# Optimization experiments

Measured on AMD Instinct MI355X. Metric: run time of the kernel, lower is better.

The kernel has to match this reference:

```python
import jax, jax.numpy as jnp
import numpy as np

BUCKETS = 16


def conv2d(x, w, b):
    # x: [N, Cin, H, W], w: [Cout, Cin, kh, kw], stride 1, padding 1
    y = jax.lax.conv_general_dilated(
        x, w, window_strides=(1, 1), padding=((1, 1), (1, 1)),
        dimension_numbers=("NCHW", "OIHW", "NCHW"))
    return y + b[None, :, None, None]


def setup_inputs() -> dict:
    key = jax.random.key(0)
    k1, k2, k3, k4, k5 = jax.random.split(key, 5)
    x = jax.random.normal(k1, (32, 64, 112, 112), dtype=jnp.float32)
    W = jax.random.normal(k2, (128, 64, 3, 3), dtype=jnp.float32) * 0.05
    b = jax.random.normal(k3, (128,), dtype=jnp.float32) * 0.05
    b2 = jax.random.normal(k4, (128,), dtype=jnp.float32) * 0.05  # hashed_conv's own bias
    hashed_weights = jax.random.normal(k5, (BUCKETS,), dtype=jnp.float32)
    return {"x": x, "W": W, "b": b, "b2": b2, "hashed_weights": hashed_weights}


def reference(x, W, b, b2, hashed_weights):
    out = conv2d(x, W, b)
    # thresholds derived from min/max of the ORIGINAL weights
    wmax = jnp.max(W)
    wmin = jnp.min(W)
    step = (wmax - wmin) / BUCKETS
    # sequential per-bucket replacement (faithful to in-place loop semantics:
    # values replaced at bucket i are re-compared against later thresholds)
    hw = W
    for i in range(BUCKETS):
        thr = (i + 1) * step + wmin
        hw = jnp.where(hw > thr, hashed_weights[i], hw)
    hashed_out = conv2d(x, hw, b2)
    return (out, hashed_out)
```

## Files before the change

### kernel.cpp

```cpp
#include <hip/hip_runtime.h>
#include <stdint.h>

#define CIN 64
#define HHW 112
#define NPIX 12544
#define COUT 128
#define KTOT 576
#define NBUCKETS 16

typedef __attribute__((ext_vector_type(8))) short s8v;
typedef __attribute__((ext_vector_type(4))) float f4v;
typedef __attribute__((ext_vector_type(8))) unsigned short u8v;

__device__ __forceinline__ unsigned short f2bf(float f) {
  unsigned int u = __float_as_uint(f);
  unsigned int r = (u + 0x7fffu + ((u >> 16) & 1u)) >> 16;
  return (unsigned short)r;
}

__device__ __forceinline__ void gload_lds16(const void* g, void* l) {
  __builtin_amdgcn_global_load_lds(
      (const __attribute__((address_space(1))) unsigned int*)g,
      (__attribute__((address_space(3))) unsigned int*)l, 16, 0, 0);
}

__global__ __launch_bounds__(1024) void hashedconv_prep_kernel(
    const float* __restrict__ W, const float* __restrict__ hashed_w,
    unsigned short* __restrict__ W2) {
  const int NW = COUT * CIN * 9;
  int tid = threadIdx.x;
  float vmin = 1e30f, vmax = -1e30f;
  for (int i = tid; i < NW; i += 1024) {
    float v = W[i];
    vmin = fminf(vmin, v);
    vmax = fmaxf(vmax, v);
  }
  #pragma unroll
  for (int off = 32; off > 0; off >>= 1) {
    vmin = fminf(vmin, __shfl_down(vmin, off, 64));
    vmax = fmaxf(vmax, __shfl_down(vmax, off, 64));
  }
  __shared__ float smin[16], smax[16];
  __shared__ float s_wmin, s_step;
  __shared__ float hv[NBUCKETS];
  int wave = tid >> 6, lane = tid & 63;
  if (lane == 0) { smin[wave] = vmin; smax[wave] = vmax; }
  if (tid < NBUCKETS) hv[tid] = hashed_w[tid];
  __syncthreads();
  if (tid == 0) {
    float m = smin[0], M = smax[0];
    #pragma unroll
    for (int i = 1; i < 16; ++i) { m = fminf(m, smin[i]); M = fmaxf(M, smax[i]); }
    s_wmin = m;
    s_step = (M - m) / (float)NBUCKETS;
  }
  __syncthreads();
  float wmin = s_wmin, step = s_step;
  for (int i = tid; i < NW; i += 1024) {
    float v = W[i];
    int co  = i / 576;
    int rem = i - co * 576;
    int cin = rem / 9;
    int off = rem - cin * 9;
    float h = v;
    #pragma unroll
    for (int b = 0; b < NBUCKETS; ++b) {
      float thr = (float)(b + 1) * step + wmin;
      if (h > thr) h = hv[b];
    }
    int oidx = co * KTOT + off * 64 + cin;
    W2[oidx]               = f2bf(v);
    W2[COUT * KTOT + oidx] = f2bf(h);
  }
}

__global__ __launch_bounds__(256) void xpose_kernel(
    const float* __restrict__ x, unsigned short* __restrict__ xb) {
  __shared__ unsigned short t[64][264];
  const int n = blockIdx.y, p0 = blockIdx.x * 256, tid = threadIdx.x;
  const float* xp = x + (size_t)n * CIN * NPIX + p0;
  #pragma unroll
  for (int c = 0; c < 64; ++c)
    t[c][tid] = f2bf(xp[(size_t)c * NPIX + tid]);
  __syncthreads();
  unsigned short* ob = xb + ((size_t)n * NPIX + p0) * 64;
  #pragma unroll
  for (int it = 0; it < 8; ++it) {
    int u = it * 256 + tid;
    int px = u >> 3, slot = u & 7;
    u8v v;
    #pragma unroll
    for (int k = 0; k < 8; ++k) v[k] = t[slot * 8 + k][px];
    *(u8v*)(ob + (size_t)u * 8) = v;
  }
}

#define XS_PIXPAD 352
#define XS_SHORTS (XS_PIXPAD * 64)
#define WS_SHORTS (COUT * 64)

__global__ __launch_bounds__(256, 2) void hashedconv_mfma_kernel(
    const unsigned short* __restrict__ xb, const unsigned short* __restrict__ W2,
    const float* __restrict__ b, const float* __restrict__ b2,
    const unsigned short* __restrict__ zp, float* __restrict__ out,
    size_t out_half) {
  __shared__ __attribute__((aligned(16))) short lds[XS_SHORTS + 2 * WS_SHORTS];
  short* xs = lds;
  short* ws0 = lds + XS_SHORTS;

  const int tid = threadIdx.x;
  const int bx = blockIdx.x;
  const int n  = blockIdx.y;
  const int hf = blockIdx.z;
  const int ty = bx / 7, tx = bx - ty * 7;
  const int h0 = ty * 16, w0 = tx * 16;
  const int lane = tid & 63, wv = tid >> 6;
  const int wr = wv >> 1, wcn = wv & 1;
  const int lrow = lane & 15, g = lane >> 4;

  const unsigned short* Wh = W2 + (size_t)hf * COUT * KTOT;

  #pragma unroll
  for (int it = 0; it < 11; ++it) {
    int u = it * 256 + tid;
    int pix = u >> 3, slot = u & 7;
    int py = pix / 18, px = pix - py * 18;
    int gh = h0 - 1 + py, gw = w0 - 1 + px;
    bool inb = (pix < 324) & (gh >= 0) & (gh < HHW) & (gw >= 0) & (gw < HHW);
    int srcslot = slot ^ (pix & 7);
    const unsigned short* gsrc = inb
        ? xb + (((size_t)n * NPIX + gh * HHW + gw) * 64 + srcslot * 8)
        : zp + srcslot * 8;
    gload_lds16(gsrc, xs + (size_t)(it * 256 + wv * 64) * 8);
  }

  auto stage_w = [&](short* buf, int c) {
    #pragma unroll
    for (int j = 0; j < 4; ++j) {
      int u = j * 256 + tid;
      int row = u >> 3, slot = u & 7;
      int srcslot = slot ^ (row & 7);
      gload_lds16(Wh + (size_t)row * KTOT + c * 64 + srcslot * 8,
                  buf + (size_t)(j * 256 + wv * 64) * 8);
    }
  };

  f4v acc[4][8];
  #pragma unroll
  for (int i = 0; i < 4; ++i)
    #pragma unroll
    for (int j = 0; j < 8; ++j) acc[i][j] = (f4v)(0.f);

  int pyv[8], pxv[8];
  #pragma unroll
  for (int nt = 0; nt < 8; ++nt) {
    int p = wcn * 128 + nt * 16 + lrow;
    pyv[nt] = p >> 4; pxv[nt] = p & 15;
  }

  stage_w(ws0, 0);
  __syncthreads();

  int cur = 0;
  for (int c = 0; c < 9; ++c) {
    short* wbuf = ws0 + cur * WS_SHORTS;
    if (c < 8) stage_w(ws0 + (cur ^ 1) * WS_SHORTS, c + 1);
    int dh = c / 3, dw = c - dh * 3;
    #pragma unroll
    for (int kh2 = 0; kh2 < 2; ++kh2) {
      int kofs = kh2 * 32 + g * 8;
      s8v af[4], bfv[8];
      #pragma unroll
      for (int mt = 0; mt < 4; ++mt) {
        int row = wr * 64 + mt * 16 + lrow;
        af[mt] = *(const s8v*)(wbuf + row * 64 + (kofs ^ ((row & 7) << 3)));
      }
      #pragma unroll
      for (int nt = 0; nt < 8; ++nt) {
        int s = (pyv[nt] + dh) * 18 + pxv[nt] + dw;
        bfv[nt] = *(const s8v*)(xs + s * 64 + (kofs ^ ((s & 7) << 3)));
      }
      #pragma unroll
      for (int mt = 0; mt < 4; ++mt)
        #pragma unroll
        for (int nt = 0; nt < 8; ++nt)
          acc[mt][nt] = __builtin_amdgcn_mfma_f32_16x16x32_bf16(
              af[mt], bfv[nt], acc[mt][nt], 0, 0, 0);
    }
    __syncthreads();
    cur ^= 1;
  }

  const float* bias = hf ? b2 : b;
  float* obase = out + (size_t)hf * out_half + (size_t)n * COUT * NPIX;
  #pragma unroll
  for (int mt = 0; mt < 4; ++mt) {
    #pragma unroll
    for (int r = 0; r < 4; ++r) {
      int co = wr * 64 + mt * 16 + g * 4 + r;
      float bv = bias[co];
      #pragma unroll
      for (int nt = 0; nt < 8; ++nt) {
        int p = wcn * 128 + nt * 16 + lrow;
        int h = h0 + (p >> 4), w = w0 + (p & 15);
        obase[(size_t)co * NPIX + h * HHW + w] = acc[mt][nt][r] + bv;
      }
    }
  }
}

__global__ __launch_bounds__(256) void hashedconv_fb_kernel(
    const float* __restrict__ x, const unsigned short* __restrict__ W2,
    const float* __restrict__ b, const float* __restrict__ b2,
    float* __restrict__ out, size_t out_half) {
  __shared__ __attribute__((aligned(16))) short lds[11520 + 8192];
  short* xs = lds;
  short* wcs = lds + 11520;
  const int tid = threadIdx.x;
  const int bx = blockIdx.x;
  const int n  = blockIdx.y;
  const int hf = blockIdx.z;
  const int ty = bx / 7, tx = bx - ty * 7;
  const int h0 = ty * 8, w0 = tx * 16;
  const int lane = tid & 63, wv = tid >> 6;
  const int wr = wv >> 1, wcn = wv & 1;
  const int lrow = lane & 15, g = lane >> 4;
  f4v acc[4][4];
  #pragma unroll
  for (int i = 0; i < 4; ++i)
    #pragma unroll
    for (int j = 0; j < 4; ++j) acc[i][j] = (f4v)(0.f);
  const float* xn = x + (size_t)n * CIN * NPIX;
  for (int u = tid; u < 1440; u += 256) {
    int cg = u / 180;
    int pix = u - cg * 180;
    int pyp = pix / 18, pxp = pix - pyp * 18;
    int gh = h0 - 1 + pyp, gw = w0 - 1 + pxp;
    bool inb = (gh >= 0) & (gh < HHW) & (gw >= 0) & (gw < HHW);
    const float* xp = xn + (size_t)(cg * 8) * NPIX + gh * HHW + gw;
    s8v pk;
    #pragma unroll
    for (int cc = 0; cc < 8; ++cc) {
      float v = inb ? xp[(size_t)cc * NPIX] : 0.f;
      pk[cc] = (short)f2bf(v);
    }
    *(s8v*)(xs + pix * 64 + ((cg * 8) ^ ((pix & 7) << 3))) = pk;
  }
  const unsigned short* Wh = W2 + (size_t)hf * COUT * KTOT;
  for (int c = 0; c < 9; ++c) {
    #pragma unroll
    for (int j = 0; j < 4; ++j) {
      int u = tid + j * 256;
      int row = u >> 3, slot = u & 7;
      s8v v = *(const s8v*)(Wh + (size_t)row * KTOT + c * 64 + slot * 8);
      *(s8v*)(wcs + row * 64 + ((slot * 8) ^ ((row & 7) << 3))) = v;
    }
    __syncthreads();
    int dh = c / 3, dw = c - dh * 3;
    #pragma unroll
    for (int kh2 = 0; kh2 < 2; ++kh2) {
      int kofs = kh2 * 32 + g * 8;
      s8v af[4], bfv[4];
      #pragma unroll
      for (int mt = 0; mt < 4; ++mt) {
        int row = wr * 64 + mt * 16 + lrow;
        af[mt] = *(const s8v*)(wcs + row * 64 + (kofs ^ ((row & 7) << 3)));
      }
      #pragma unroll
      for (int nt = 0; nt < 4; ++nt) {
        int p = wcn * 64 + nt * 16 + lrow;
        int s = ((p >> 4) + dh) * 18 + ((p & 15) + dw);
        bfv[nt] = *(const s8v*)(xs + s * 64 + (kofs ^ ((s & 7) << 3)));
      }
      #pragma unroll
      for (int mt = 0; mt < 4; ++mt)
        #pragma unroll
        for (int nt = 0; nt < 4; ++nt)
          acc[mt][nt] = __builtin_amdgcn_mfma_f32_16x16x32_bf16(
              af[mt], bfv[nt], acc[mt][nt], 0, 0, 0);
    }
    __syncthreads();
  }
  const float* bias = hf ? b2 : b;
  float* obase = out + (size_t)hf * out_half + (size_t)n * COUT * NPIX;
  #pragma unroll
  for (int mt = 0; mt < 4; ++mt) {
    #pragma unroll
    for (int r = 0; r < 4; ++r) {
      int co = wr * 64 + mt * 16 + g * 4 + r;
      float bv = bias[co];
      #pragma unroll
      for (int nt = 0; nt < 4; ++nt) {
        int p = wcn * 64 + nt * 16 + lrow;
        int h = h0 + (p >> 4), w = w0 + (p & 15);
        obase[(size_t)co * NPIX + h * HHW + w] = acc[mt][nt][r] + bv;
      }
    }
  }
}

extern "C" void kernel_launch(void* const* d_in, const int* in_sizes, int n_in,
                              void* d_out, int out_size, void* d_ws, size_t ws_size,
                              hipStream_t stream) {
  const float* x      = (const float*)d_in[0];
  const float* W      = (const float*)d_in[1];
  const float* b      = (const float*)d_in[2];
  const float* b2     = (const float*)d_in[3];
  const float* hashed = (const float*)d_in[4];
  float* out = (float*)d_out;

  const int N = in_sizes[0] / (CIN * NPIX);
  const size_t out_half = (size_t)N * COUT * NPIX;
  const size_t XB_SHORTS = (size_t)N * NPIX * 64;
  const size_t need = (XB_SHORTS + 2 * COUT * KTOT) * 2 + 256;

  if (ws_size >= need) {
    unsigned short* xb = (unsigned short*)d_ws;
    unsigned short* W2 = xb + XB_SHORTS;
    unsigned short* zp = W2 + 2 * COUT * KTOT;
    hipMemsetAsync(zp, 0, 256, stream);
    hipLaunchKernelGGL(hashedconv_prep_kernel, dim3(1), dim3(1024), 0, stream,
                       W, hashed, W2);
    hipLaunchKernelGGL(xpose_kernel, dim3(NPIX / 256, N), dim3(256), 0, stream,
                       x, xb);
    hipLaunchKernelGGL(hashedconv_mfma_kernel, dim3(49, N, 2), dim3(256), 0,
                       stream, xb, W2, b, b2, zp, out, out_half);
  } else {
    unsigned short* W2 = (unsigned short*)d_ws;
    hipLaunchKernelGGL(hashedconv_prep_kernel, dim3(1), dim3(1024), 0, stream,
                       W, hashed, W2);
    hipLaunchKernelGGL(hashedconv_fb_kernel, dim3(98, N, 2), dim3(256), 0,
                       stream, x, W2, b, b2, out, out_half);
  }
}
```

Baseline: 274.0 us.

## Merge both conv outputs into one 512-thread block sharing the input tile

The separate z-dimension launch for the two weight sets is replaced by a single 512-thread block that computes all 256 output channels (original and hashed) against one staged input tile. This halves input-tile global loads and LDS staging per output. The K loop now uses explicit barriers, waitcnt and setprio around the MFMA bursts. The zero-pad memset is folded into the prep kernel, which removes one API call. In exchange, LDS use per block roughly doubles and accumulator registers per wave change, which may cut occupancy.

```diff
diff --git a/kernel.cpp b/kernel.cpp
--- a/kernel.cpp
+++ b/kernel.cpp
@@ -26,9 +26,10 @@
 
 __global__ __launch_bounds__(1024) void hashedconv_prep_kernel(
     const float* __restrict__ W, const float* __restrict__ hashed_w,
-    unsigned short* __restrict__ W2) {
+    unsigned short* __restrict__ W2, unsigned short* __restrict__ zp) {
   const int NW = COUT * CIN * 9;
   int tid = threadIdx.x;
+  if (zp && tid < 128) zp[tid] = 0;
   float vmin = 1e30f, vmax = -1e30f;
   for (int i = tid; i < NW; i += 1024) {
     float v = W[i];
@@ -95,34 +96,32 @@
   }
 }
 
-#define XS_PIXPAD 352
+#define XS_PIXPAD 384
 #define XS_SHORTS (XS_PIXPAD * 64)
-#define WS_SHORTS (COUT * 64)
-
-__global__ __launch_bounds__(256, 2) void hashedconv_mfma_kernel(
+#define WS_SHORTS (256 * 64)
+
+__global__ __launch_bounds__(512, 2) void hashedconv_mfma_kernel(
     const unsigned short* __restrict__ xb, const unsigned short* __restrict__ W2,
     const float* __restrict__ b, const float* __restrict__ b2,
     const unsigned short* __restrict__ zp, float* __restrict__ out,
     size_t out_half) {
   __shared__ __attribute__((aligned(16))) short lds[XS_SHORTS + 2 * WS_SHORTS];
   short* xs = lds;
-  short* ws0 = lds + XS_SHORTS;
+  short* wb0 = lds + XS_SHORTS;
 
   const int tid = threadIdx.x;
   const int bx = blockIdx.x;
   const int n  = blockIdx.y;
-  const int hf = blockIdx.z;
   const int ty = bx / 7, tx = bx - ty * 7;
   const int h0 = ty * 16, w0 = tx * 16;
   const int lane = tid & 63, wv = tid >> 6;
-  const int wr = wv >> 1, wcn = wv & 1;
+  const int wr = wv >> 2;
+  const int wcn = wv & 3;
   const int lrow = lane & 15, g = lane >> 4;
 
-  const unsigned short* Wh = W2 + (size_t)hf * COUT * KTOT;
-
-  #pragma unroll
-  for (int it = 0; it < 11; ++it) {
-    int u = it * 256 + tid;
+  #pragma unroll
+  for (int it = 0; it < 6; ++it) {
+    int u = it * 512 + tid;
     int pix = u >> 3, slot = u & 7;
     int py = pix / 18, px = pix - py * 18;
     int gh = h0 - 1 + py, gw = w0 - 1 + px;
@@ -131,77 +130,110 @@
     const unsigned short* gsrc = inb
         ? xb + (((size_t)n * NPIX + gh * HHW + gw) * 64 + srcslot * 8)
         : zp + srcslot * 8;
-    gload_lds16(gsrc, xs + (size_t)(it * 256 + wv * 64) * 8);
+    gload_lds16(gsrc, xs + (size_t)(it * 512 + wv * 64) * 8);
   }
 
   auto stage_w = [&](short* buf, int c) {
     #pragma unroll
     for (int j = 0; j < 4; ++j) {
-      int u = j * 256 + tid;
+      int u = j * 512 + tid;
       int row = u >> 3, slot = u & 7;
       int srcslot = slot ^ (row & 7);
-      gload_lds16(Wh + (size_t)row * KTOT + c * 64 + srcslot * 8,
-                  buf + (size_t)(j * 256 + wv * 64) * 8);
+      gload_lds16(W2 + (size_t)row * KTOT + c * 64 + srcslot * 8,
+                  buf + (size_t)(j * 512 + wv * 64) * 8);
     }
   };
-
-  f4v acc[4][8];
-  #pragma unroll
-  for (int i = 0; i < 4; ++i)
-    #pragma unroll
-    for (int j = 0; j < 8; ++j) acc[i][j] = (f4v)(0.f);
-
-  int pyv[8], pxv[8];
-  #pragma unroll
-  for (int nt = 0; nt < 8; ++nt) {
-    int p = wcn * 128 + nt * 16 + lrow;
+  stage_w(wb0, 0);
+  __syncthreads();
+
+  f4v acc[8][4];
+  #pragma unroll
+  for (int i = 0; i < 8; ++i)
+    #pragma unroll
+    for (int j = 0; j < 4; ++j) acc[i][j] = (f4v)(0.f);
+
+  int pyv[4], pxv[4];
+  #pragma unroll
+  for (int nt = 0; nt < 4; ++nt) {
+    int p = wcn * 64 + nt * 16 + lrow;
     pyv[nt] = p >> 4; pxv[nt] = p & 15;
   }
 
-  stage_w(ws0, 0);
-  __syncthreads();
-
-  int cur = 0;
   for (int c = 0; c < 9; ++c) {
-    short* wbuf = ws0 + cur * WS_SHORTS;
-    if (c < 8) stage_w(ws0 + (cur ^ 1) * WS_SHORTS, c + 1);
-    int dh = c / 3, dw = c - dh * 3;
-    #pragma unroll
-    for (int kh2 = 0; kh2 < 2; ++kh2) {
-      int kofs = kh2 * 32 + g * 8;
-      s8v af[4], bfv[8];
-      #pragma unroll
-      for (int mt = 0; mt < 4; ++mt) {
-        int row = wr * 64 + mt * 16 + lrow;
-        af[mt] = *(const s8v*)(wbuf + row * 64 + (kofs ^ ((row & 7) << 3)));
-      }
-      #pragma unroll
-      for (int nt = 0; nt < 8; ++nt) {
+    short* wb = wb0 + (c & 1) * WS_SHORTS;
+    const int dh = c / 3, dw = c - dh * 3;
+
+    if (c < 8) stage_w(wb0 + ((c + 1) & 1) * WS_SHORTS, c + 1);
+    {
+      const int kofs = g * 8;
+      s8v af[8], bfv[4];
+      #pragma unroll
+      for (int mt = 0; mt < 8; ++mt) {
+        int row = wr * 128 + mt * 16 + lrow;
+        af[mt] = *(const s8v*)(wb + row * 64 + (kofs ^ ((row & 7) << 3)));
+      }
+      #pragma unroll
+      for (int nt = 0; nt < 4; ++nt) {
         int s = (pyv[nt] + dh) * 18 + pxv[nt] + dw;
         bfv[nt] = *(const s8v*)(xs + s * 64 + (kofs ^ ((s & 7) << 3)));
       }
-      #pragma unroll
-      for (int mt = 0; mt < 4; ++mt)
+      __builtin_amdgcn_sched_barrier(0);
+      __builtin_amdgcn_s_barrier();
+      asm volatile("s_waitcnt lgkmcnt(0)");
+      __builtin_amdgcn_sched_barrier(0);
+      __builtin_amdgcn_s_setprio(1);
+      #pragma unroll
+      for (int mt = 0; mt < 8; ++mt)
         #pragma unroll
-        for (int nt = 0; nt < 8; ++nt)
+        for (int nt = 0; nt < 4; ++nt)
           acc[mt][nt] = __builtin_amdgcn_mfma_f32_16x16x32_bf16(
               af[mt], bfv[nt], acc[mt][nt], 0, 0, 0);
-    }
-    __syncthreads();
-    cur ^= 1;
-  }
-
-  const float* bias = hf ? b2 : b;
-  float* obase = out + (size_t)hf * out_half + (size_t)n * COUT * NPIX;
-  #pragma unroll
-  for (int mt = 0; mt < 4; ++mt) {
+      __builtin_amdgcn_s_setprio(0);
+      __builtin_amdgcn_sched_barrier(0);
+      __builtin_amdgcn_s_barrier();
+    }
+    {
+      const int kofs = 32 + g * 8;
+      s8v af[8], bfv[4];
+      #pragma unroll
+      for (int mt = 0; mt < 8; ++mt) {
+        int row = wr * 128 + mt * 16 + lrow;
+        af[mt] = *(const s8v*)(wb + row * 64 + (kofs ^ ((row & 7) << 3)));
+      }
+      #pragma unroll
+      for (int nt = 0; nt < 4; ++nt) {
+        int s = (pyv[nt] + dh) * 18 + pxv[nt] + dw;
+        bfv[nt] = *(const s8v*)(xs + s * 64 + (kofs ^ ((s & 7) << 3)));
+      }
+      __builtin_amdgcn_sched_barrier(0);
+      __builtin_amdgcn_s_barrier();
+      asm volatile("s_waitcnt lgkmcnt(0)");
+      __builtin_amdgcn_sched_barrier(0);
+      __builtin_amdgcn_s_setprio(1);
+      #pragma unroll
+      for (int mt = 0; mt < 8; ++mt)
+        #pragma unroll
+        for (int nt = 0; nt < 4; ++nt)
+          acc[mt][nt] = __builtin_amdgcn_mfma_f32_16x16x32_bf16(
+              af[mt], bfv[nt], acc[mt][nt], 0, 0, 0);
+      __builtin_amdgcn_s_setprio(0);
+      __builtin_amdgcn_sched_barrier(0);
+      asm volatile("s_waitcnt vmcnt(0)");
+      __builtin_amdgcn_s_barrier();
+    }
+  }
+
+  const float* bias = wr ? b2 : b;
+  float* obase = out + (size_t)wr * out_half + (size_t)n * COUT * NPIX;
+  #pragma unroll
+  for (int mt = 0; mt < 8; ++mt) {
     #pragma unroll
     for (int r = 0; r < 4; ++r) {
-      int co = wr * 64 + mt * 16 + g * 4 + r;
+      int co = (mt * 16 + g * 4 + r) & 127;
       float bv = bias[co];
       #pragma unroll
-      for (int nt = 0; nt < 8; ++nt) {
-        int p = wcn * 128 + nt * 16 + lrow;
+      for (int nt = 0; nt < 4; ++nt) {
+        int p = wcn * 64 + nt * 16 + lrow;
         int h = h0 + (p >> 4), w = w0 + (p & 15);
         obase[(size_t)co * NPIX + h * HHW + w] = acc[mt][nt][r] + bv;
       }
@@ -318,17 +350,16 @@
     unsigned short* xb = (unsigned short*)d_ws;
     unsigned short* W2 = xb + XB_SHORTS;
     unsigned short* zp = W2 + 2 * COUT * KTOT;
-    hipMemsetAsync(zp, 0, 256, stream);
     hipLaunchKernelGGL(hashedconv_prep_kernel, dim3(1), dim3(1024), 0, stream,
-                       W, hashed, W2);
+                       W, hashed, W2, zp);
     hipLaunchKernelGGL(xpose_kernel, dim3(NPIX / 256, N), dim3(256), 0, stream,
                        x, xb);
-    hipLaunchKernelGGL(hashedconv_mfma_kernel, dim3(49, N, 2), dim3(256), 0,
+    hipLaunchKernelGGL(hashedconv_mfma_kernel, dim3(49, N), dim3(512), 0,
                        stream, xb, W2, b, b2, zp, out, out_half);
   } else {
     unsigned short* W2 = (unsigned short*)d_ws;
     hipLaunchKernelGGL(hashedconv_prep_kernel, dim3(1), dim3(1024), 0, stream,
-                       W, hashed, W2);
+                       W, hashed, W2, (unsigned short*)nullptr);
     hipLaunchKernelGGL(hashedconv_fb_kernel, dim3(98, N, 2), dim3(256), 0,
                        stream, x, W2, b, b2, out, out_half);
   }
```

Measured after the change: 330.5 us. 1.21x slower.
